# Kernel optimization log

Hardware: AMD Instinct MI355X
Metric: run time of the kernel (lower is better)

The kernel has to match this reference:

```python
import jax, jax.numpy as jnp
import numpy as np

NUM_CLASSES = 3
IMG = 448
STRIDES = (8, 16, 32)
POS_IOU, NEG_IOU = 0.5, 0.3
NEG_RATIO = 3
B, T = 64, 20


def _make_anchors(stride):
    f = IMG // stride
    cs = (np.arange(f, dtype=np.float32) + 0.5) * stride
    cx, cy = np.meshgrid(cs, cs, indexing='xy')            # [f, f]
    sizes = np.array([2.0, 2.5, 3.0], np.float32) * stride  # 3 square anchors / loc
    cx = np.broadcast_to(cx[..., None], (f, f, 3))
    cy = np.broadcast_to(cy[..., None], (f, f, 3))
    w = np.broadcast_to(sizes, (f, f, 3))
    boxes = np.stack([cx - w / 2, cy - w / 2, cx + w / 2, cy + w / 2], -1)
    return jnp.asarray(boxes.reshape(-1, 4), jnp.float32)   # [f*f*3, 4]


def setup_inputs() -> dict:
    key = jax.random.key(0)
    k1, k2, k3, kc, ks, kl = jax.random.split(key, 6)
    pred1 = jax.random.normal(k1, (B, 24, 56, 56), jnp.float32)
    pred2 = jax.random.normal(k2, (B, 24, 28, 28), jnp.float32)
    pred3 = jax.random.normal(k3, (B, 24, 14, 14), jnp.float32)
    ctr = jax.random.uniform(kc, (B, T, 2), jnp.float32, 20.0, IMG - 20.0)
    wh = jax.random.uniform(ks, (B, T, 2), jnp.float32, 20.0, 120.0)
    target_boxes = jnp.concatenate([ctr - wh / 2, ctr + wh / 2], axis=-1)  # [B,T,4] xyxy
    target_labels = jax.random.randint(kl, (B, T), 1, NUM_CLASSES + 1, jnp.int32)
    return {
        'pred1': pred1, 'pred2': pred2, 'pred3': pred3,
        'anchor1': _make_anchors(8), 'anchor2': _make_anchors(16), 'anchor3': _make_anchors(32),
        'target_boxes': target_boxes, 'target_labels': target_labels,
    }


def _iou(a, b):  # a [A,4], b [T,4] -> [A,T]
    lt = jnp.maximum(a[:, None, :2], b[None, :, :2])
    rb = jnp.minimum(a[:, None, 2:], b[None, :, 2:])
    wh = jnp.clip(rb - lt, 0.0)
    inter = wh[..., 0] * wh[..., 1]
    area_a = (a[:, 2] - a[:, 0]) * (a[:, 3] - a[:, 1])
    area_b = (b[:, 2] - b[:, 0]) * (b[:, 3] - b[:, 1])
    return inter / (area_a[:, None] + area_b[None, :] - inter + 1e-9)


def _encode(gt, an):  # both [A,4] xyxy -> [A,4] deltas
    aw, ah = an[:, 2] - an[:, 0], an[:, 3] - an[:, 1]
    acx, acy = (an[:, 0] + an[:, 2]) * 0.5, (an[:, 1] + an[:, 3]) * 0.5
    gw, gh = gt[:, 2] - gt[:, 0], gt[:, 3] - gt[:, 1]
    gcx, gcy = (gt[:, 0] + gt[:, 2]) * 0.5, (gt[:, 1] + gt[:, 3]) * 0.5
    return jnp.stack([(gcx - acx) / aw, (gcy - acy) / ah,
                      jnp.log(gw / aw), jnp.log(gh / ah)], axis=-1)


def _bce_logits(x, y):
    return jnp.maximum(x, 0.0) - x * y + jnp.log1p(jnp.exp(-jnp.abs(x)))


def _image_loss(deltas, obj, cls, boxes, labels, anchors):
    # deltas [A,4], obj [A], cls [A,K], boxes [T,4], labels [T], anchors [A,4]
    iou = _iou(anchors, boxes)                    # [A,T]
    matched_t = jnp.argmax(iou, axis=1)           # [A]
    max_iou = jnp.max(iou, axis=1)
    pos = max_iou >= POS_IOU
    neg = max_iou < NEG_IOU
    # force each GT's best anchor to be positive
    best_a = jnp.argmax(iou, axis=0)              # [T]
    matched_t = matched_t.at[best_a].set(jnp.arange(boxes.shape[0]))
    pos = pos.at[best_a].set(True)
    neg = neg.at[best_a].set(False)
    matched_labels = jnp.where(pos, labels[matched_t], 0)
    # objectness + hard negative mining (rank-based topk, jit-safe)
    obj_t = (matched_labels > 0).astype(obj.dtype)
    bce = _bce_logits(obj, obj_t)
    num_pos = pos.sum()
    need = jnp.minimum(NEG_RATIO * num_pos, neg.sum())
    rank = jnp.argsort(jnp.argsort(-jnp.where(neg, bce, -jnp.inf)))
    sel = pos | ((rank < need) & neg)
    obj_loss = jnp.sum(jnp.where(sel, bce, 0.0)) / jnp.maximum(sel.sum(), 1)
    # classification (mean over positives)
    logp = jax.nn.log_softmax(cls, axis=-1)
    tgt = jnp.maximum(matched_labels - 1, 0)
    ce = -jnp.take_along_axis(logp, tgt[:, None], axis=1)[:, 0]
    cls_loss = jnp.sum(jnp.where(pos, ce, 0.0)) / jnp.maximum(num_pos, 1)
    # localization: smooth L1, mean over positive anchor elements
    tdel = _encode(boxes[matched_t], anchors)
    d = jnp.abs(deltas - tdel)
    sl1 = jnp.where(d < 1.0, 0.5 * d * d, d - 0.5)
    loc_loss = jnp.sum(jnp.where(pos[:, None], sl1, 0.0)) / jnp.maximum(4 * num_pos, 1)
    return obj_loss, cls_loss, loc_loss


def _scale_loss(pred, anchors, boxes, labels):
    Bp, C, H, W = pred.shape
    p = pred.transpose(0, 2, 3, 1).reshape(Bp, H * W * 3, 5 + NUM_CLASSES)
    deltas, obj, cls = p[..., :4], p[..., 4], p[..., 5:]
    fn = jax.vmap(lambda d, o, c, b, l: _image_loss(d, o, c, b, l, anchors))
    ol, cl, ll = fn(deltas, obj, cls, boxes, labels)
    return ol.sum(), cl.sum(), ll.sum()


def reference(pred1, pred2, pred3, anchor1, anchor2, anchor3, target_boxes, target_labels):
    tot = jnp.zeros(3, jnp.float32)
    for pred, anc in ((pred1, anchor1), (pred2, anchor2), (pred3, anchor3)):
        ol, cl, ll = _scale_loss(pred, anc, target_boxes, target_labels)
        tot = tot + jnp.stack([ol, cl, ll])
    bsz = target_boxes.shape[0]
    obj, cls, loc = tot[0] / bsz, tot[1] / bsz, tot[2] / bsz
    total = obj + cls + 2.0 * loc
    return jnp.stack([obj, cls, loc, total])
```

## Files before the change

kernel.cpp:

```cpp
#include <hip/hip_runtime.h>
#include <math.h>

#define T 20
#define APB 12348
#define NPNN_OFF 64
#define KEY_OFF  256
#define MF_BYTE_OFF (4 * (KEY_OFF + 64 * APB))

__device__ __forceinline__ unsigned mapf(float x) {
    unsigned u = __float_as_uint(x);
    return (u & 0x80000000u) ? ~u : (u | 0x80000000u);
}
__device__ __forceinline__ float unmapf(unsigned m) {
    return __uint_as_float((m & 0x80000000u) ? (m ^ 0x80000000u) : ~m);
}
__device__ __forceinline__ float bce_pos(float x) {
    return fmaxf(x, 0.f) - x + log1pf(expf(-fabsf(x)));
}
__device__ __forceinline__ float bce_neg(float x) {
    return fmaxf(x, 0.f) + log1pf(expf(-fabsf(x)));
}

__global__ __launch_bounds__(256) void match_kernel(
    const float* __restrict__ pred1, const float* __restrict__ pred2,
    const float* __restrict__ pred3, const float* __restrict__ tboxes,
    unsigned* __restrict__ wsu, unsigned short* __restrict__ mf)
{
#pragma clang fp contract(off)
    const int blk = blockIdx.x;
    const int b = blk / 11, c = blk - 11 * b;
    int s, j0;
    if (c < 8)       { s = 0; j0 = c * 1176; }
    else if (c < 10) { s = 1; j0 = (c - 8) * 1176; }
    else             { s = 2; j0 = 0; }
    const float* __restrict__ pred = (s == 0) ? pred1 : (s == 1) ? pred2 : pred3;
    const int W = 56 >> s, HW = W * W, A = 3 * HW;
    const float stf = (float)(8 << s);
    const int sh = 3 - s;
    const int lim = min(1176, A - j0);

    __shared__ float4 s_box[T];
    __shared__ float  s_ab[T];
    const int tid = threadIdx.x, lane = tid & 63;

    if (tid < T) {
        float4 g = ((const float4*)tboxes)[b * T + tid];
        s_box[tid] = g;
        s_ab[tid]  = (g.z - g.x) * (g.w - g.y);
    }
    __syncthreads();

    float ax[5], ay[5], az[5], aw[5], ar[5], bn[5], bu[5];
    int at_[5], jj[5];
#pragma unroll
    for (int q = 0; q < 5; q++) {
        int o = tid + q * 256;
        int j = j0 + ((o < lim) ? o : 0);
        jj[q] = j;
        int k   = (j >= HW) + (j >= 2 * HW);
        int pix = j - k * HW;
        int qq  = pix >> sh;
        int py  = (qq * 9363) >> 16;
        int px  = pix - py * W;
        float w  = (2.0f + 0.5f * (float)k) * stf;
        float cx = ((float)px + 0.5f) * stf;
        float cy = ((float)py + 0.5f) * stf;
        ax[q] = cx - 0.5f * w; ay[q] = cy - 0.5f * w;
        az[q] = cx + 0.5f * w; aw[q] = cy + 0.5f * w;
        ar[q] = w * w;
        bn[q] = -1.f; bu[q] = 1.f; at_[q] = 0;
    }
    for (int t = 0; t < T; t++) {
        float4 g = s_box[t];
        float  ab = s_ab[t];
#pragma unroll
        for (int q = 0; q < 5; q++) {
            float lx = fmaxf(ax[q], g.x), ly = fmaxf(ay[q], g.y);
            float rx = fminf(az[q], g.z), ry = fminf(aw[q], g.w);
            float ww = fmaxf(rx - lx, 0.f), hh = fmaxf(ry - ly, 0.f);
            float inter = ww * hh;
            float u = ((ar[q] + ab) - inter) + 1e-9f;
            if (inter * bu[q] > bn[q] * u) { bn[q] = inter; bu[q] = u; at_[q] = t; }
        }
    }

    const float* objbase = pred + (size_t)(b * 24 + 4) * HW;
    const unsigned base = (unsigned)(b * APB + ((s == 0) ? 0 : (s == 1) ? 9408 : 11760));
    unsigned npnn = 0;
#pragma unroll
    for (int q = 0; q < 5; q++) {
        int o = tid + q * 256;
        if (o < lim) {
            int j = jj[q];
            int k   = (j >= HW) + (j >= 2 * HW);
            int pix = j - k * HW;
            bool pos = (bn[q] + bn[q] >= bu[q]);
            bool neg = (bn[q] < 0.3f * bu[q]);
            float x = objbase[(size_t)k * 8 * HW + pix];
            wsu[KEY_OFF + base + j] = neg ? mapf(x) : 0u;
            mf[base + j] = (unsigned short)(at_[q] | (pos ? 0x100 : 0) | (neg ? 0x200 : 0));
            npnn += (pos ? 1u : 0u) + (neg ? 0x10000u : 0u);
        }
    }
    for (int off = 32; off; off >>= 1) npnn += (unsigned)__shfl_down((int)npnn, off, 64);
    if (lane == 0) atomicAdd(&wsu[NPNN_OFF + b * 3 + s], npnn);
}

__global__ __launch_bounds__(1024) void select_loss_kernel(
    const float* __restrict__ pred1, const float* __restrict__ pred2,
    const float* __restrict__ pred3, const float* __restrict__ tboxes,
    const int* __restrict__ tlabels,
    unsigned* __restrict__ wsu, unsigned short* __restrict__ mf,
    float* __restrict__ acc)
{
#pragma clang fp contract(off)
    const int bid = blockIdx.x;
    const int b = bid / 3, s = bid - 3 * b;
    const float* __restrict__ pred = (s == 0) ? pred1 : (s == 1) ? pred2 : pred3;
    const int W = 56 >> s, HW = W * W, A = 3 * HW;
    const float stf = (float)(8 << s);
    const int sh = 3 - s;
    const unsigned base = (unsigned)(b * APB + ((s == 0) ? 0 : (s == 1) ? 9408 : 11760));

    __shared__ float4   s_box[T];
    __shared__ int      s_lab[T];
    __shared__ int      s_besta[T];
    __shared__ unsigned s_cnt[33];
    __shared__ float    s_redf[16 * 4];

    const int tid = threadIdx.x, lane = tid & 63, wid = tid >> 6;

    if (tid < T) {
        s_box[tid] = ((const float4*)tboxes)[b * T + tid];
        s_lab[tid] = tlabels[b * T + tid];
    }
    if (tid >= 64 && tid < 64 + 33) s_cnt[tid - 64] = 0;
    __syncthreads();

    for (int t = wid; t < T; t += 16) {
        float4 g = s_box[t];
        float  ab = (g.z - g.x) * (g.w - g.y);
        int px0 = max(0, (int)floorf(g.x / stf) - 2);
        int px1 = min(W - 1, (int)floorf(g.z / stf) + 2);
        int py0 = max(0, (int)floorf(g.y / stf) - 2);
        int py1 = min(W - 1, (int)floorf(g.w / stf) + 2);
        int rowlen = (px1 - px0 + 1) * 3;
        float bi = -1.f, bu2 = 1.f;
        int ba = 0;
        for (int py = py0; py <= py1; py++) {
            float cy = ((float)py + 0.5f) * stf;
            for (int cc = lane; cc < rowlen; cc += 64) {
                int ix = (cc * 21846) >> 16;
                int k  = cc - 3 * ix;
                int px = px0 + ix;
                float w  = (2.0f + 0.5f * (float)k) * stf;
                float cx = ((float)px + 0.5f) * stf;
                float lx = fmaxf(cx - 0.5f * w, g.x), ly = fmaxf(cy - 0.5f * w, g.y);
                float rx = fminf(cx + 0.5f * w, g.z), ry = fminf(cy + 0.5f * w, g.w);
                float ww = fmaxf(rx - lx, 0.f), hh = fmaxf(ry - ly, 0.f);
                float inter = ww * hh;
                float u = ((w * w + ab) - inter) + 1e-9f;
                if (inter * bu2 > bi * u) {
                    bi = inter; bu2 = u; ba = (py * W + px) * 3 + k;
                }
            }
        }
        for (int off = 32; off; off >>= 1) {
            float oi = __shfl_down(bi, off, 64);
            float ou = __shfl_down(bu2, off, 64);
            int   oa = __shfl_down(ba, off, 64);
            float l = oi * bu2, r = bi * ou;
            if (l > r || (l == r && oa < ba)) { bi = oi; bu2 = ou; ba = oa; }
        }
        if (lane == 0) s_besta[t] = ba;
    }
    __syncthreads();

    int  j20 = 0; bool winner = false;
    if (tid < T) {
        int a = s_besta[tid];
        winner = true; bool first = true;
        for (int t2 = tid + 1; t2 < T; t2++) if (s_besta[t2] == a) winner = false;
        for (int t2 = 0; t2 < tid; t2++)     if (s_besta[t2] == a) first  = false;
        int pix = (a * 21846) >> 16;
        int k = a - 3 * pix;
        j20 = k * HW + pix;
        if (first) {
            unsigned old = mf[base + j20];
            unsigned d = ((old & 0x100u) ? 0u : 1u) +
                         ((old & 0x200u) ? 0xFFFF0000u : 0u);
            atomicAdd(&s_cnt[32], d);
        }
    }
    __syncthreads();
    if (tid < T && winner) {
        mf[base + j20] = (unsigned short)(tid | 0x100);
        wsu[KEY_OFF + base + j20] = 0u;
    }
    __threadfence_block();
    __syncthreads();

    unsigned packed = wsu[NPNN_OFF + bid] + s_cnt[32];
    unsigned np = packed & 0xFFFFu, nn = packed >> 16;
    unsigned need = min(3u * np, nn);

    unsigned keyreg[10];
#pragma unroll
    for (int m = 0; m < 10; m++) {
        int j = tid + m * 1024;
        keyreg[m] = (j < A) ? wsu[KEY_OFF + base + j] : 0u;
    }

    unsigned kth = 0xFFFFFFFFu;
    if (need > 0) {
        unsigned lo = 0u, hi = 0xFFFFFFFFu;
        int it = 0;
        while (lo < hi) {
            unsigned d = hi - lo;
            unsigned mid = lo + (d >> 1) + (d & 1u);
            unsigned cnt = 0;
#pragma unroll
            for (int m = 0; m < 10; m++) cnt += (keyreg[m] >= mid) ? 1u : 0u;
            for (int off = 32; off; off >>= 1) cnt += (unsigned)__shfl_down((int)cnt, off, 64);
            if (lane == 0) atomicAdd(&s_cnt[it], cnt);
            __syncthreads();
            cnt = s_cnt[it]; it++;
            if (cnt >= need) lo = mid; else hi = mid - 1;
        }
        kth = lo;
    }

    float obj_s = 0.f, cls_s = 0.f, loc_s = 0.f;
    unsigned cgt = 0;
#pragma unroll 1
    for (int m = 0; m < 10; m++) {
        int j = tid + m * 1024;
        if (j >= A) break;
        unsigned mfv = mf[base + j];
        if (mfv & 0x100u) {
            int k   = (j >= HW) + (j >= 2 * HW);
            int pix = j - k * HW;
            const float* bp = pred + (size_t)(b * 24 + k * 8) * HW + pix;
            float x = bp[(size_t)4 * HW];
            obj_s += bce_pos(x);
            int t = mfv & 0xFFu;
            float4 g = s_box[t];
            int tgt = s_lab[t] - 1;
            float c0 = bp[(size_t)5 * HW], c1 = bp[(size_t)6 * HW], c2 = bp[(size_t)7 * HW];
            float mm  = fmaxf(c0, fmaxf(c1, c2));
            float lse = logf(expf(c0 - mm) + expf(c1 - mm) + expf(c2 - mm));
            float ct = (tgt == 0) ? c0 : (tgt == 1) ? c1 : c2;
            cls_s += (mm + lse) - ct;
            int qq = pix >> sh;
            int py = (qq * 9363) >> 16;
            int px = pix - py * W;
            float w  = (2.0f + 0.5f * (float)k) * stf;
            float cx = ((float)px + 0.5f) * stf;
            float cy = ((float)py + 0.5f) * stf;
            float gcx = (g.x + g.z) * 0.5f, gcy = (g.y + g.w) * 0.5f;
            float gw = g.z - g.x, gh = g.w - g.y;
            float t0 = (gcx - cx) / w, t1 = (gcy - cy) / w;
            float t2 = logf(gw / w),   t3 = logf(gh / w);
            float d0 = bp[0], d1 = bp[(size_t)HW], d2 = bp[(size_t)2 * HW], d3 = bp[(size_t)3 * HW];
            float dd;
            dd = fabsf(d0 - t0); loc_s += (dd < 1.f) ? 0.5f * dd * dd : dd - 0.5f;
            dd = fabsf(d1 - t1); loc_s += (dd < 1.f) ? 0.5f * dd * dd : dd - 0.5f;
            dd = fabsf(d2 - t2); loc_s += (dd < 1.f) ? 0.5f * dd * dd : dd - 0.5f;
            dd = fabsf(d3 - t3); loc_s += (dd < 1.f) ? 0.5f * dd * dd : dd - 0.5f;
        } else {
            unsigned key = keyreg[m];
            if (key > kth) { obj_s += bce_neg(unmapf(key)); cgt++; }
        }
    }
    for (int off = 32; off; off >>= 1) {
        obj_s += __shfl_down(obj_s, off, 64);
        cls_s += __shfl_down(cls_s, off, 64);
        loc_s += __shfl_down(loc_s, off, 64);
        cgt   += (unsigned)__shfl_down((int)cgt, off, 64);
    }
    if (lane == 0) {
        s_redf[wid * 4 + 0] = obj_s;
        s_redf[wid * 4 + 1] = cls_s;
        s_redf[wid * 4 + 2] = loc_s;
        s_redf[wid * 4 + 3] = __uint_as_float(cgt);
    }
    __syncthreads();
    if (tid == 0) {
        float ob = 0.f, cl = 0.f, lc = 0.f;
        unsigned cg = 0;
        for (int w2 = 0; w2 < 16; w2++) {
            ob += s_redf[w2 * 4 + 0];
            cl += s_redf[w2 * 4 + 1];
            lc += s_redf[w2 * 4 + 2];
            cg += __float_as_uint(s_redf[w2 * 4 + 3]);
        }
        if (need > 0) ob += (float)(need - cg) * bce_neg(unmapf(kth));
        atomicAdd(acc + 0, ob / (float)max(np + need, 1u));
        atomicAdd(acc + 1, cl / (float)max(np, 1u));
        atomicAdd(acc + 2, lc / (float)max(4u * np, 1u));
    }
}

__global__ void init_kernel(unsigned* __restrict__ wsu) {
    int tid = threadIdx.x;
    if (tid < 3) ((float*)wsu)[tid] = 0.f;
    if (tid >= NPNN_OFF && tid < NPNN_OFF + 192) wsu[tid] = 0u;
}

__global__ void finalize_kernel(const float* __restrict__ acc,
                                float* __restrict__ out) {
    if (threadIdx.x == 0) {
        float obj = acc[0] / 64.f;
        float cls = acc[1] / 64.f;
        float loc = acc[2] / 64.f;
        out[0] = obj;
        out[1] = cls;
        out[2] = loc;
        out[3] = obj + cls + 2.f * loc;
    }
}

extern "C" void kernel_launch(void* const* d_in, const int* in_sizes, int n_in,
                              void* d_out, int out_size, void* d_ws, size_t ws_size,
                              hipStream_t stream) {
    const float* pred1   = (const float*)d_in[0];
    const float* pred2   = (const float*)d_in[1];
    const float* pred3   = (const float*)d_in[2];
    const float* tboxes  = (const float*)d_in[6];
    const int*   tlabels = (const int*)d_in[7];
    unsigned* wsu = (unsigned*)d_ws;
    unsigned short* mf = (unsigned short*)((char*)d_ws + MF_BYTE_OFF);
    float* acc = (float*)d_ws;
    float* out = (float*)d_out;

    init_kernel<<<1, 256, 0, stream>>>(wsu);
    match_kernel<<<64 * 11, 256, 0, stream>>>(pred1, pred2, pred3, tboxes, wsu, mf);
    select_loss_kernel<<<64 * 3, 1024, 0, stream>>>(
        pred1, pred2, pred3, tboxes, tlabels, wsu, mf, acc);
    finalize_kernel<<<1, 64, 0, stream>>>(acc, out);
}
```

Measured before the change: 139.5 us.

## Replace bisection top-k with radix histogram select and drop init kernel

The 32-step binary search for the k-th largest negative key becomes a three-pass radix select that uses shared-memory histograms. The match kernel now gives each thread contiguous anchors, skips targets whose boxes miss the thread's anchor bounding box, and loads the objectness value only for negatives. Per-block counts and losses go to dedicated workspace slots instead of global atomics, so the init kernel is removed and finalize does a parallel reduction. The mask read is hoisted into registers. The bounding-box skip relies on a zero initial best IoU so that skipped targets match the old result, and the radix passes add shared-memory atomics and extra barriers.

Result: faster. 124.3 us (-10.9%).

```diff
diff --git a/kernel.cpp b/kernel.cpp
--- a/kernel.cpp
+++ b/kernel.cpp
@@ -3,8 +3,9 @@
 
 #define T 20
 #define APB 12348
-#define NPNN_OFF 64
-#define KEY_OFF  256
+#define LOSS_OFF 16
+#define NPNN_OFF 640
+#define KEY_OFF  2048
 #define MF_BYTE_OFF (4 * (KEY_OFF + 64 * APB))
 
 __device__ __forceinline__ unsigned mapf(float x) {
@@ -39,9 +40,10 @@
     const int sh = 3 - s;
     const int lim = min(1176, A - j0);
 
-    __shared__ float4 s_box[T];
-    __shared__ float  s_ab[T];
-    const int tid = threadIdx.x, lane = tid & 63;
+    __shared__ float4   s_box[T];
+    __shared__ float    s_ab[T];
+    __shared__ unsigned s_np[4];
+    const int tid = threadIdx.x, lane = tid & 63, wid = tid >> 6;
 
     if (tid < T) {
         float4 g = ((const float4*)tboxes)[b * T + tid];
@@ -51,12 +53,15 @@
     __syncthreads();
 
     float ax[5], ay[5], az[5], aw[5], ar[5], bn[5], bu[5];
-    int at_[5], jj[5];
-#pragma unroll
-    for (int q = 0; q < 5; q++) {
-        int o = tid + q * 256;
-        int j = j0 + ((o < lim) ? o : 0);
-        jj[q] = j;
+    int at_[5], kk[5], pp[5];
+    bool vv[5];
+    float xlo = 1e30f, xhi = -1e30f, ylo = 1e30f, yhi = -1e30f;
+    const int obase = 5 * tid;
+#pragma unroll
+    for (int r = 0; r < 5; r++) {
+        int o = obase + r;
+        vv[r] = (o < lim);
+        int j = j0 + (vv[r] ? o : 0);
         int k   = (j >= HW) + (j >= 2 * HW);
         int pix = j - k * HW;
         int qq  = pix >> sh;
@@ -65,22 +70,28 @@
         float w  = (2.0f + 0.5f * (float)k) * stf;
         float cx = ((float)px + 0.5f) * stf;
         float cy = ((float)py + 0.5f) * stf;
-        ax[q] = cx - 0.5f * w; ay[q] = cy - 0.5f * w;
-        az[q] = cx + 0.5f * w; aw[q] = cy + 0.5f * w;
-        ar[q] = w * w;
-        bn[q] = -1.f; bu[q] = 1.f; at_[q] = 0;
-    }
+        ax[r] = cx - 0.5f * w; ay[r] = cy - 0.5f * w;
+        az[r] = cx + 0.5f * w; aw[r] = cy + 0.5f * w;
+        ar[r] = w * w;
+        bn[r] = 0.f; bu[r] = 1.f; at_[r] = 0;
+        kk[r] = k; pp[r] = pix;
+        xlo = fminf(xlo, ax[r]); xhi = fmaxf(xhi, az[r]);
+        ylo = fminf(ylo, ay[r]); yhi = fmaxf(yhi, aw[r]);
+    }
+
     for (int t = 0; t < T; t++) {
         float4 g = s_box[t];
-        float  ab = s_ab[t];
-#pragma unroll
-        for (int q = 0; q < 5; q++) {
-            float lx = fmaxf(ax[q], g.x), ly = fmaxf(ay[q], g.y);
-            float rx = fminf(az[q], g.z), ry = fminf(aw[q], g.w);
-            float ww = fmaxf(rx - lx, 0.f), hh = fmaxf(ry - ly, 0.f);
-            float inter = ww * hh;
-            float u = ((ar[q] + ab) - inter) + 1e-9f;
-            if (inter * bu[q] > bn[q] * u) { bn[q] = inter; bu[q] = u; at_[q] = t; }
+        if (g.x < xhi && g.z > xlo && g.y < yhi && g.w > ylo) {
+            float ab = s_ab[t];
+#pragma unroll
+            for (int r = 0; r < 5; r++) {
+                float lx = fmaxf(ax[r], g.x), ly = fmaxf(ay[r], g.y);
+                float rx = fminf(az[r], g.z), ry = fminf(aw[r], g.w);
+                float ww = fmaxf(rx - lx, 0.f), hh = fmaxf(ry - ly, 0.f);
+                float inter = ww * hh;
+                float u = ((ar[r] + ab) - inter) + 1e-9f;
+                if (inter * bu[r] > bn[r] * u) { bn[r] = inter; bu[r] = u; at_[r] = t; }
+            }
         }
     }
 
@@ -88,30 +99,29 @@
     const unsigned base = (unsigned)(b * APB + ((s == 0) ? 0 : (s == 1) ? 9408 : 11760));
     unsigned npnn = 0;
 #pragma unroll
-    for (int q = 0; q < 5; q++) {
-        int o = tid + q * 256;
-        if (o < lim) {
-            int j = jj[q];
-            int k   = (j >= HW) + (j >= 2 * HW);
-            int pix = j - k * HW;
-            bool pos = (bn[q] + bn[q] >= bu[q]);
-            bool neg = (bn[q] < 0.3f * bu[q]);
-            float x = objbase[(size_t)k * 8 * HW + pix];
-            wsu[KEY_OFF + base + j] = neg ? mapf(x) : 0u;
-            mf[base + j] = (unsigned short)(at_[q] | (pos ? 0x100 : 0) | (neg ? 0x200 : 0));
+    for (int r = 0; r < 5; r++) {
+        if (vv[r]) {
+            int j = j0 + obase + r;
+            bool pos = (bn[r] + bn[r] >= bu[r]);
+            bool neg = (bn[r] < 0.3f * bu[r]);
+            unsigned key = 0u;
+            if (neg) key = mapf(objbase[(size_t)kk[r] * 8 * HW + pp[r]]);
+            wsu[KEY_OFF + base + j] = key;
+            mf[base + j] = (unsigned short)(at_[r] | (pos ? 0x100 : 0) | (neg ? 0x200 : 0));
             npnn += (pos ? 1u : 0u) + (neg ? 0x10000u : 0u);
         }
     }
     for (int off = 32; off; off >>= 1) npnn += (unsigned)__shfl_down((int)npnn, off, 64);
-    if (lane == 0) atomicAdd(&wsu[NPNN_OFF + b * 3 + s], npnn);
+    if (lane == 0) s_np[wid] = npnn;
+    __syncthreads();
+    if (tid == 0) wsu[NPNN_OFF + blk] = s_np[0] + s_np[1] + s_np[2] + s_np[3];
 }
 
 __global__ __launch_bounds__(1024) void select_loss_kernel(
     const float* __restrict__ pred1, const float* __restrict__ pred2,
     const float* __restrict__ pred3, const float* __restrict__ tboxes,
     const int* __restrict__ tlabels,
-    unsigned* __restrict__ wsu, unsigned short* __restrict__ mf,
-    float* __restrict__ acc)
+    unsigned* __restrict__ wsu, unsigned short* __restrict__ mf)
 {
 #pragma clang fp contract(off)
     const int bid = blockIdx.x;
@@ -125,8 +135,9 @@
     __shared__ float4   s_box[T];
     __shared__ int      s_lab[T];
     __shared__ int      s_besta[T];
-    __shared__ unsigned s_cnt[33];
+    __shared__ unsigned s_misc[4];
     __shared__ float    s_redf[16 * 4];
+    __shared__ unsigned hist[2048];
 
     const int tid = threadIdx.x, lane = tid & 63, wid = tid >> 6;
 
@@ -134,7 +145,7 @@
         s_box[tid] = ((const float4*)tboxes)[b * T + tid];
         s_lab[tid] = tlabels[b * T + tid];
     }
-    if (tid >= 64 && tid < 64 + 33) s_cnt[tid - 64] = 0;
+    if (tid >= 32 && tid < 36) s_misc[tid - 32] = 0;
     __syncthreads();
 
     for (int t = wid; t < T; t += 16) {
@@ -189,7 +200,7 @@
             unsigned old = mf[base + j20];
             unsigned d = ((old & 0x100u) ? 0u : 1u) +
                          ((old & 0x200u) ? 0xFFFF0000u : 0u);
-            atomicAdd(&s_cnt[32], d);
+            atomicAdd(&s_misc[0], d);
         }
     }
     __syncthreads();
@@ -200,34 +211,70 @@
     __threadfence_block();
     __syncthreads();
 
-    unsigned packed = wsu[NPNN_OFF + bid] + s_cnt[32];
+    if (tid == 0) {
+        int nslots = (s == 0) ? 8 : (s == 1) ? 2 : 1;
+        int sb = b * 11 + ((s == 0) ? 0 : (s == 1) ? 8 : 10);
+        unsigned p = 0;
+        for (int i = 0; i < nslots; i++) p += wsu[NPNN_OFF + sb + i];
+        s_misc[1] = p;
+    }
+    __syncthreads();
+    unsigned packed = s_misc[1] + s_misc[0];
     unsigned np = packed & 0xFFFFu, nn = packed >> 16;
     unsigned need = min(3u * np, nn);
 
     unsigned keyreg[10];
+    unsigned short mfr[10];
 #pragma unroll
     for (int m = 0; m < 10; m++) {
         int j = tid + m * 1024;
         keyreg[m] = (j < A) ? wsu[KEY_OFF + base + j] : 0u;
+        mfr[m]    = (j < A) ? mf[base + j] : (unsigned short)0;
     }
 
     unsigned kth = 0xFFFFFFFFu;
     if (need > 0) {
-        unsigned lo = 0u, hi = 0xFFFFFFFFu;
-        int it = 0;
-        while (lo < hi) {
-            unsigned d = hi - lo;
-            unsigned mid = lo + (d >> 1) + (d & 1u);
-            unsigned cnt = 0;
-#pragma unroll
-            for (int m = 0; m < 10; m++) cnt += (keyreg[m] >= mid) ? 1u : 0u;
-            for (int off = 32; off; off >>= 1) cnt += (unsigned)__shfl_down((int)cnt, off, 64);
-            if (lane == 0) atomicAdd(&s_cnt[it], cnt);
+        unsigned prefix = 0, remaining = need;
+        const int shifts[3] = {21, 10, 0};
+        const int nbits[3]  = {11, 11, 10};
+        for (int p = 0; p < 3; p++) {
+            const int NB = 1 << nbits[p];
+            const int sh_ = shifts[p];
+            for (int i = tid; i < NB; i += 1024) hist[i] = 0;
             __syncthreads();
-            cnt = s_cnt[it]; it++;
-            if (cnt >= need) lo = mid; else hi = mid - 1;
-        }
-        kth = lo;
+#pragma unroll
+            for (int m = 0; m < 10; m++) {
+                unsigned k = keyreg[m];
+                bool ok = (p == 0) || ((k >> (sh_ + nbits[p])) == prefix);
+                if (ok) atomicAdd(&hist[(k >> sh_) & (NB - 1)], 1u);
+            }
+            __syncthreads();
+            if (wid == 0) {
+                const int C = NB >> 6;
+                int b0 = lane * C;
+                unsigned csum = 0;
+                for (int i = 0; i < C; i++) csum += hist[b0 + i];
+                unsigned Tv = csum;
+                for (int off = 1; off < 64; off <<= 1) {
+                    unsigned o = __shfl_down(Tv, off, 64);
+                    if (lane + off < 64) Tv += o;
+                }
+                unsigned long long ball = __ballot(Tv >= remaining);
+                int L = 63 - __clzll(ball);
+                if (lane == L) {
+                    unsigned sv = Tv - csum;
+                    int bb = b0 + C - 1;
+                    while (true) { sv += hist[bb]; if (sv >= remaining) break; bb--; }
+                    s_misc[1] = (unsigned)bb;
+                    s_misc[2] = sv - hist[bb];
+                }
+            }
+            __syncthreads();
+            unsigned B = s_misc[1];
+            remaining -= s_misc[2];
+            prefix = (prefix << nbits[p]) | B;
+        }
+        kth = prefix;
     }
 
     float obj_s = 0.f, cls_s = 0.f, loc_s = 0.f;
@@ -236,7 +283,7 @@
     for (int m = 0; m < 10; m++) {
         int j = tid + m * 1024;
         if (j >= A) break;
-        unsigned mfv = mf[base + j];
+        unsigned mfv = mfr[m];
         if (mfv & 0x100u) {
             int k   = (j >= HW) + (j >= 2 * HW);
             int pix = j - k * HW;
@@ -295,27 +342,37 @@
             cg += __float_as_uint(s_redf[w2 * 4 + 3]);
         }
         if (need > 0) ob += (float)(need - cg) * bce_neg(unmapf(kth));
-        atomicAdd(acc + 0, ob / (float)max(np + need, 1u));
-        atomicAdd(acc + 1, cl / (float)max(np, 1u));
-        atomicAdd(acc + 2, lc / (float)max(4u * np, 1u));
-    }
-}
-
-__global__ void init_kernel(unsigned* __restrict__ wsu) {
-    int tid = threadIdx.x;
-    if (tid < 3) ((float*)wsu)[tid] = 0.f;
-    if (tid >= NPNN_OFF && tid < NPNN_OFF + 192) wsu[tid] = 0u;
-}
-
-__global__ void finalize_kernel(const float* __restrict__ acc,
+        float* wsf = (float*)wsu;
+        wsf[LOSS_OFF + bid * 3 + 0] = ob / (float)max(np + need, 1u);
+        wsf[LOSS_OFF + bid * 3 + 1] = cl / (float)max(np, 1u);
+        wsf[LOSS_OFF + bid * 3 + 2] = lc / (float)max(4u * np, 1u);
+    }
+}
+
+__global__ void finalize_kernel(const float* __restrict__ wsf,
                                 float* __restrict__ out) {
-    if (threadIdx.x == 0) {
-        float obj = acc[0] / 64.f;
-        float cls = acc[1] / 64.f;
-        float loc = acc[2] / 64.f;
-        out[0] = obj;
-        out[1] = cls;
-        out[2] = loc;
+    const int t = threadIdx.x, lane = t & 63, wid = t >> 6;
+    __shared__ float red[12];
+    float v0 = 0.f, v1 = 0.f, v2 = 0.f;
+    if (t < 192) {
+        v0 = wsf[LOSS_OFF + 3 * t];
+        v1 = wsf[LOSS_OFF + 3 * t + 1];
+        v2 = wsf[LOSS_OFF + 3 * t + 2];
+    }
+    for (int off = 32; off; off >>= 1) {
+        v0 += __shfl_down(v0, off, 64);
+        v1 += __shfl_down(v1, off, 64);
+        v2 += __shfl_down(v2, off, 64);
+    }
+    if (lane == 0) { red[wid * 3] = v0; red[wid * 3 + 1] = v1; red[wid * 3 + 2] = v2; }
+    __syncthreads();
+    if (t == 0) {
+        float obj = 0.f, cls = 0.f, loc = 0.f;
+        for (int w2 = 0; w2 < 4; w2++) {
+            obj += red[w2 * 3]; cls += red[w2 * 3 + 1]; loc += red[w2 * 3 + 2];
+        }
+        obj /= 64.f; cls /= 64.f; loc /= 64.f;
+        out[0] = obj; out[1] = cls; out[2] = loc;
         out[3] = obj + cls + 2.f * loc;
     }
 }
@@ -330,12 +387,10 @@
     const int*   tlabels = (const int*)d_in[7];
     unsigned* wsu = (unsigned*)d_ws;
     unsigned short* mf = (unsigned short*)((char*)d_ws + MF_BYTE_OFF);
-    float* acc = (float*)d_ws;
     float* out = (float*)d_out;
 
-    init_kernel<<<1, 256, 0, stream>>>(wsu);
     match_kernel<<<64 * 11, 256, 0, stream>>>(pred1, pred2, pred3, tboxes, wsu, mf);
     select_loss_kernel<<<64 * 3, 1024, 0, stream>>>(
-        pred1, pred2, pred3, tboxes, tlabels, wsu, mf, acc);
-    finalize_kernel<<<1, 64, 0, stream>>>(acc, out);
-}
+        pred1, pred2, pred3, tboxes, tlabels, wsu, mf);
+    finalize_kernel<<<1, 256, 0, stream>>>((const float*)d_ws, out);
+}
```
